# Kernel optimization log

Hardware: AMD Instinct MI355X
Metric: run time of the kernel (lower is better)

## Reference

```python
import jax, jax.numpy as jnp
import numpy as np

WINDOW_SIZE = 5
SIGMA = 1.5


def gaussian_kernel_3d(size, sigma):
    # Faithful replication of the torch code (including its permute quirk):
    # kernel[i,j,k] = exp(-((k-off)^2 + (k-off)^2 + (i-off)^2) / (2*sigma^2))
    c = jnp.arange(size, dtype=jnp.float32) - size // 2
    ci = c[:, None, None]  # axis 0 term (from permute(2,0,1))
    ck = c[None, None, :]  # axis 2 term (coords and permute(1,0,2) coincide)
    g = jnp.exp(-(ck ** 2 + ck ** 2 + ci ** 2) / (2.0 * sigma ** 2))
    g = jnp.broadcast_to(g, (size, size, size))
    return g / g.sum()


def _conv3d(x, w, pad):
    # x: [N,C,D,H,W], w: [O,I,kd,kh,kw]
    return jax.lax.conv_general_dilated(
        x, w, window_strides=(1, 1, 1),
        padding=[(pad, pad)] * 3,
        dimension_numbers=('NCDHW', 'OIDHW', 'NCDHW'))


def setup_inputs() -> dict:
    key = jax.random.key(0)
    k1, k2 = jax.random.split(key)
    img1 = jax.random.uniform(k1, (4, 2, 128, 128, 128), dtype=jnp.float32)
    img2 = jax.random.uniform(k2, (4, 1, 128, 128, 128), dtype=jnp.float32)
    window = gaussian_kernel_3d(WINDOW_SIZE, SIGMA)[None, None]  # [1,1,5,5,5]
    return {"img1": img1, "img2": img2, "window": window}


def reference(img1, img2, window):
    ws = window.shape[-1]
    pad = ws // 2
    x1 = img1[:, 1:2]  # select channel 1, keep dim -> [B,1,D,H,W]
    x2 = img2
    mu1 = _conv3d(x1, window, pad)
    mu2 = _conv3d(x2, window, pad)
    mu1_sq = mu1 * mu1
    mu2_sq = mu2 * mu2
    mu1_mu2 = mu1 * mu2
    sigma1_sq = _conv3d(x1 * x1, window, pad) - mu1_sq
    sigma2_sq = _conv3d(x2 * x2, window, pad) - mu2_sq
    sigma12 = _conv3d(x1 * x2, window, pad) - mu1_mu2
    C1 = 0.01 ** 2
    C2 = 0.03 ** 2
    ssim_map = ((2.0 * mu1_mu2 + C1) * (2.0 * sigma12 + C2)) / (
        (mu1_sq + mu2_sq + C1) * (sigma1_sq + sigma2_sq + C2))
    return 1.0 - jnp.mean(ssim_map)
```

## Files before the change

### kernel.cpp

```cpp
#include <hip/hip_runtime.h>


#define NDIM 128
#define TH 4
#define WR (TH + 4)
#define DSUB 16
#define NHT (NDIM / TH)
#define NDT (NDIM / DSUB)
#define NB 4
#define NBLK (NHT * NDT * NB)

__global__ void factorize_window(const float* __restrict__ w, float* __restrict__ ws) {
    if (threadIdx.x == 0) {
        float w000 = w[0];
        #pragma unroll
        for (int i = 0; i < 5; ++i) ws[i]      = w[i * 25];
        #pragma unroll
        for (int j = 0; j < 5; ++j) ws[5 + j]  = w[j * 5] / w000;
        #pragma unroll
        for (int k = 0; k < 5; ++k) ws[10 + k] = w[k] / w000;
    }
}

__launch_bounds__(256, 4)
__global__ void ssim_main(const float* __restrict__ img1,
                          const float* __restrict__ img2,
                          const float* __restrict__ wfac,
                          float* __restrict__ partials) {
    const int bid = blockIdx.x;
    const int th = bid % NHT;
    const int td = (bid / NHT) % NDT;
    const int b  = bid / (NHT * NDT);

    const int h0 = th * TH, d0 = td * DSUB;
    const float* __restrict__ x1 = img1 + (size_t)(b * 2 + 1) * NDIM * NDIM * NDIM;
    const float* __restrict__ x2 = img2 + (size_t)b * NDIM * NDIM * NDIM;

    float uW[5], vW[5], tW[5];
    #pragma unroll
    for (int i = 0; i < 5; ++i) { uW[i] = wfac[i]; vW[i] = wfac[5 + i]; tW[i] = wfac[10 + i]; }

    __shared__ float sWc[5][WR][NDIM];
    __shared__ float sRed[4];

    const int tid  = threadIdx.x;
    const int wrow = tid >> 5;
    const int wcg  = tid & 31;
    const int c0   = wcg * 4;
    const int ghw  = h0 + wrow - 2;
    const int orow = tid >> 6;
    const int oc   = (tid & 63) * 2;

    float2 ring[5][5];
    float2 accS = make_float2(0.f, 0.f);

#define PHASE(I, P) do {                                                       \
    const int i_ = (I);                                                        \
    const int d_ = d0 - 2 + i_;                                                \
    float4 A0 = make_float4(0,0,0,0), A1 = A0, A2 = A0;                        \
    float4 B0 = A0, B1 = A0, B2 = A0;                                          \
    if (((unsigned)d_ < NDIM) && ((unsigned)ghw < NDIM)) {                     \
        const float* __restrict__ r1_ = x1 + ((size_t)d_ * NDIM + ghw) * NDIM; \
        const float* __restrict__ r2_ = x2 + ((size_t)d_ * NDIM + ghw) * NDIM; \
        if (wcg > 0)  { A0 = *(const float4*)(r1_ + c0 - 4);                   \
                        B0 = *(const float4*)(r2_ + c0 - 4); }                 \
        A1 = *(const float4*)(r1_ + c0);                                       \
        B1 = *(const float4*)(r2_ + c0);                                       \
        if (wcg < 31) { A2 = *(const float4*)(r1_ + c0 + 4);                   \
                        B2 = *(const float4*)(r2_ + c0 + 4); }                 \
    }                                                                          \
    float ra[12] = {A0.x,A0.y,A0.z,A0.w, A1.x,A1.y,A1.z,A1.w,                  \
                    A2.x,A2.y,A2.z,A2.w};                                      \
    float rb[12] = {B0.x,B0.y,B0.z,B0.w, B1.x,B1.y,B1.z,B1.w,                  \
                    B2.x,B2.y,B2.z,B2.w};                                      \
    float m1v[4], m2v[4], q11v[4], q22v[4], q12v[4];                           \
    _Pragma("unroll")                                                          \
    for (int k_ = 0; k_ < 4; ++k_) {                                           \
        float m1_=0.f, m2_=0.f, q11_=0.f, q22_=0.f, q12_=0.f;                  \
        _Pragma("unroll")                                                      \
        for (int c_ = 0; c_ < 5; ++c_) {                                       \
            const float a_ = ra[k_ + c_ + 2], b_ = rb[k_ + c_ + 2];            \
            const float ta_ = tW[c_] * a_, tb_ = tW[c_] * b_;                  \
            m1_ += ta_; m2_ += tb_;                                            \
            q11_ += ta_ * a_; q22_ += tb_ * b_; q12_ += ta_ * b_;              \
        }                                                                      \
        m1v[k_]=m1_; m2v[k_]=m2_; q11v[k_]=q11_; q22v[k_]=q22_; q12v[k_]=q12_; \
    }                                                                          \
    __syncthreads();                   \
    *(float4*)&sWc[0][wrow][c0] = make_float4(m1v[0],m1v[1],m1v[2],m1v[3]);    \
    *(float4*)&sWc[1][wrow][c0] = make_float4(m2v[0],m2v[1],m2v[2],m2v[3]);    \
    *(float4*)&sWc[2][wrow][c0] = make_float4(q11v[0],q11v[1],q11v[2],q11v[3]);\
    *(float4*)&sWc[3][wrow][c0] = make_float4(q22v[0],q22v[1],q22v[2],q22v[3]);\
    *(float4*)&sWc[4][wrow][c0] = make_float4(q12v[0],q12v[1],q12v[2],q12v[3]);\
    __syncthreads();                                       \
    _Pragma("unroll")                                                          \
    for (int f_ = 0; f_ < 5; ++f_) {                                           \
        float2 F_ = make_float2(0.f, 0.f);                                     \
        _Pragma("unroll")                                                      \
        for (int r_ = 0; r_ < 5; ++r_) {                                       \
            const float2 wv_ = *(const float2*)&sWc[f_][orow + r_][oc];        \
            F_.x += vW[r_] * wv_.x;                                            \
            F_.y += vW[r_] * wv_.y;                                            \
        }                                                                      \
        ring[(P)][f_] = F_;                                                    \
    }                                                                          \
    if (i_ >= 4) {                                                             \
        float2 F0 = make_float2(0,0), F1 = F0, F2 = F0, F3 = F0, F4 = F0;      \
        _Pragma("unroll")                                                      \
        for (int j_ = 0; j_ < 5; ++j_) {                                       \
            const int s_ = ((P) + 1 + j_) % 5;                                 \
            const float uw_ = uW[j_];                                          \
            F0.x += uw_*ring[s_][0].x; F0.y += uw_*ring[s_][0].y;              \
            F1.x += uw_*ring[s_][1].x; F1.y += uw_*ring[s_][1].y;              \
            F2.x += uw_*ring[s_][2].x; F2.y += uw_*ring[s_][2].y;              \
            F3.x += uw_*ring[s_][3].x; F3.y += uw_*ring[s_][3].y;              \
            F4.x += uw_*ring[s_][4].x; F4.y += uw_*ring[s_][4].y;              \
        }                                                                      \
        {                                                                      \
            const float mu1 = F0.x, mu2 = F1.x;                                \
            const float m11 = mu1*mu1, m22 = mu2*mu2, m12 = mu1*mu2;           \
            const float num = (2.f*m12 + 1e-4f) * (2.f*(F4.x - m12) + 9e-4f);  \
            const float den = (m11 + m22 + 1e-4f) *                            \
                              ((F2.x - m11) + (F3.x - m22) + 9e-4f);           \
            accS.x += __fdividef(num, den);                                    \
        }                                                                      \
        {                                                                      \
            const float mu1 = F0.y, mu2 = F1.y;                                \
            const float m11 = mu1*mu1, m22 = mu2*mu2, m12 = mu1*mu2;           \
            const float num = (2.f*m12 + 1e-4f) * (2.f*(F4.y - m12) + 9e-4f);  \
            const float den = (m11 + m22 + 1e-4f) *                            \
                              ((F2.y - m11) + (F3.y - m22) + 9e-4f);           \
            accS.y += __fdividef(num, den);                                    \
        }                                                                      \
    }                                                                          \
} while (0)

    for (int io = 0; io < 4; ++io) {
        const int ib = io * 5;
        PHASE(ib + 0, 0);
        PHASE(ib + 1, 1);
        PHASE(ib + 2, 2);
        PHASE(ib + 3, 3);
        PHASE(ib + 4, 4);
    }
#undef PHASE

    float acc = accS.x + accS.y;
    #pragma unroll
    for (int off = 32; off > 0; off >>= 1)
        acc += __shfl_down(acc, off, 64);
    __syncthreads();
    if ((tid & 63) == 0) sRed[tid >> 6] = acc;
    __syncthreads();
    if (tid == 0) partials[bid] = sRed[0] + sRed[1] + sRed[2] + sRed[3];
}

__global__ void finalize_kernel(const float* __restrict__ partials, float* __restrict__ out) {
    const int tid = threadIdx.x;
    double s = 0.0;
    for (int i = tid; i < NBLK; i += 256) s += (double)partials[i];
    #pragma unroll
    for (int off = 32; off > 0; off >>= 1)
        s += __shfl_down(s, off, 64);
    __shared__ double sm[4];
    if ((tid & 63) == 0) sm[tid >> 6] = s;
    __syncthreads();
    if (tid == 0)
        out[0] = 1.0f - (float)((sm[0] + sm[1] + sm[2] + sm[3]) / (double)(4LL * 128 * 128 * 128));
}

extern "C" void kernel_launch(void* const* d_in, const int* in_sizes, int n_in,
                              void* d_out, int out_size, void* d_ws, size_t ws_size,
                              hipStream_t stream) {
    const float* img1 = (const float*)d_in[0];
    const float* img2 = (const float*)d_in[1];
    const float* win  = (const float*)d_in[2];
    float* out = (float*)d_out;
    float* ws  = (float*)d_ws;
    float* wfac     = ws;
    float* partials = ws + 16;

    hipLaunchKernelGGL(factorize_window, dim3(1), dim3(64), 0, stream, win, wfac);
    hipLaunchKernelGGL(ssim_main, dim3(NBLK), dim3(256), 0, stream, img1, img2, wfac, partials);
    hipLaunchKernelGGL(finalize_kernel, dim3(1), dim3(256), 0, stream, partials, out);
}
```

Before: 162.8 us.

## Split W dimension into two 64-wide tiles per block

Adds a width tiling so each block handles 64 columns instead of 128, doubling the block count. Each thread now loads float2 instead of float4 and computes two W-filtered outputs. The H pass runs only on half the threads (tid<128). The aim is more blocks for better occupancy and latency hiding. In exchange, halo reads across tile boundaries become redundant and half the threads sit idle in the H/D stage.

```diff
diff --git a/kernel.cpp b/kernel.cpp
--- a/kernel.cpp
+++ b/kernel.cpp
@@ -2,13 +2,15 @@
 
 
 #define NDIM 128
+#define TW64 64
 #define TH 4
 #define WR (TH + 4)
 #define DSUB 16
+#define NWT 2
 #define NHT (NDIM / TH)
 #define NDT (NDIM / DSUB)
 #define NB 4
-#define NBLK (NHT * NDT * NB)
+#define NBLK (NWT * NHT * NDT * NB)
 
 __global__ void factorize_window(const float* __restrict__ w, float* __restrict__ ws) {
     if (threadIdx.x == 0) {
@@ -28,11 +30,13 @@
                           const float* __restrict__ wfac,
                           float* __restrict__ partials) {
     const int bid = blockIdx.x;
-    const int th = bid % NHT;
-    const int td = (bid / NHT) % NDT;
-    const int b  = bid / (NHT * NDT);
+    const int tw = bid % NWT;
+    int t1 = bid / NWT;
+    const int th = t1 % NHT; t1 /= NHT;
+    const int td = t1 % NDT;
+    const int b  = t1 / NDT;
 
-    const int h0 = th * TH, d0 = td * DSUB;
+    const int w0 = tw * TW64, h0 = th * TH, d0 = td * DSUB;
     const float* __restrict__ x1 = img1 + (size_t)(b * 2 + 1) * NDIM * NDIM * NDIM;
     const float* __restrict__ x2 = img2 + (size_t)b * NDIM * NDIM * NDIM;
 
@@ -40,16 +44,20 @@
     #pragma unroll
     for (int i = 0; i < 5; ++i) { uW[i] = wfac[i]; vW[i] = wfac[5 + i]; tW[i] = wfac[10 + i]; }
 
-    __shared__ float sWc[5][WR][NDIM];
+    __shared__ float sWc[5][WR][TW64];
     __shared__ float sRed[4];
 
     const int tid  = threadIdx.x;
     const int wrow = tid >> 5;
     const int wcg  = tid & 31;
-    const int c0   = wcg * 4;
+    const int lc0  = wcg * 2;
+    const int gc0  = w0 + lc0;
     const int ghw  = h0 + wrow - 2;
-    const int orow = tid >> 6;
-    const int oc   = (tid & 63) * 2;
+    const bool haveL = (gc0 >= 2);
+    const bool haveR = (gc0 <= 124);
+    const bool active = (tid < 128);
+    const int orow = tid >> 5;
+    const int oc   = (tid & 31) * 2;
 
     float2 ring[5][5];
     float2 accS = make_float2(0.f, 0.f);
@@ -57,29 +65,27 @@
 #define PHASE(I, P) do {                                                       \
     const int i_ = (I);                                                        \
     const int d_ = d0 - 2 + i_;                                                \
-    float4 A0 = make_float4(0,0,0,0), A1 = A0, A2 = A0;                        \
-    float4 B0 = A0, B1 = A0, B2 = A0;                                          \
+    float2 A0 = make_float2(0,0), A1 = A0, A2 = A0;                            \
+    float2 B0 = A0, B1 = A0, B2 = A0;                                          \
     if (((unsigned)d_ < NDIM) && ((unsigned)ghw < NDIM)) {                     \
         const float* __restrict__ r1_ = x1 + ((size_t)d_ * NDIM + ghw) * NDIM; \
         const float* __restrict__ r2_ = x2 + ((size_t)d_ * NDIM + ghw) * NDIM; \
-        if (wcg > 0)  { A0 = *(const float4*)(r1_ + c0 - 4);                   \
-                        B0 = *(const float4*)(r2_ + c0 - 4); }                 \
-        A1 = *(const float4*)(r1_ + c0);                                       \
-        B1 = *(const float4*)(r2_ + c0);                                       \
-        if (wcg < 31) { A2 = *(const float4*)(r1_ + c0 + 4);                   \
-                        B2 = *(const float4*)(r2_ + c0 + 4); }                 \
+        if (haveL) { A0 = *(const float2*)(r1_ + gc0 - 2);                     \
+                     B0 = *(const float2*)(r2_ + gc0 - 2); }                   \
+        A1 = *(const float2*)(r1_ + gc0);                                      \
+        B1 = *(const float2*)(r2_ + gc0);                                      \
+        if (haveR) { A2 = *(const float2*)(r1_ + gc0 + 2);                     \
+                     B2 = *(const float2*)(r2_ + gc0 + 2); }                   \
     }                                                                          \
-    float ra[12] = {A0.x,A0.y,A0.z,A0.w, A1.x,A1.y,A1.z,A1.w,                  \
-                    A2.x,A2.y,A2.z,A2.w};                                      \
-    float rb[12] = {B0.x,B0.y,B0.z,B0.w, B1.x,B1.y,B1.z,B1.w,                  \
-                    B2.x,B2.y,B2.z,B2.w};                                      \
-    float m1v[4], m2v[4], q11v[4], q22v[4], q12v[4];                           \
+    float ra[6] = {A0.x, A0.y, A1.x, A1.y, A2.x, A2.y};                        \
+    float rb[6] = {B0.x, B0.y, B1.x, B1.y, B2.x, B2.y};                        \
+    float m1v[2], m2v[2], q11v[2], q22v[2], q12v[2];                           \
     _Pragma("unroll")                                                          \
-    for (int k_ = 0; k_ < 4; ++k_) {                                           \
+    for (int k_ = 0; k_ < 2; ++k_) {                                           \
         float m1_=0.f, m2_=0.f, q11_=0.f, q22_=0.f, q12_=0.f;                  \
         _Pragma("unroll")                                                      \
         for (int c_ = 0; c_ < 5; ++c_) {                                       \
-            const float a_ = ra[k_ + c_ + 2], b_ = rb[k_ + c_ + 2];            \
+            const float a_ = ra[k_ + c_], b_ = rb[k_ + c_];                    \
             const float ta_ = tW[c_] * a_, tb_ = tW[c_] * b_;                  \
             m1_ += ta_; m2_ += tb_;                                            \
             q11_ += ta_ * a_; q22_ += tb_ * b_; q12_ += ta_ * b_;              \
@@ -87,50 +93,52 @@
         m1v[k_]=m1_; m2v[k_]=m2_; q11v[k_]=q11_; q22v[k_]=q22_; q12v[k_]=q12_; \
     }                                                                          \
     __syncthreads();                   \
-    *(float4*)&sWc[0][wrow][c0] = make_float4(m1v[0],m1v[1],m1v[2],m1v[3]);    \
-    *(float4*)&sWc[1][wrow][c0] = make_float4(m2v[0],m2v[1],m2v[2],m2v[3]);    \
-    *(float4*)&sWc[2][wrow][c0] = make_float4(q11v[0],q11v[1],q11v[2],q11v[3]);\
-    *(float4*)&sWc[3][wrow][c0] = make_float4(q22v[0],q22v[1],q22v[2],q22v[3]);\
-    *(float4*)&sWc[4][wrow][c0] = make_float4(q12v[0],q12v[1],q12v[2],q12v[3]);\
+    *(float2*)&sWc[0][wrow][lc0] = make_float2(m1v[0], m1v[1]);                \
+    *(float2*)&sWc[1][wrow][lc0] = make_float2(m2v[0], m2v[1]);                \
+    *(float2*)&sWc[2][wrow][lc0] = make_float2(q11v[0], q11v[1]);              \
+    *(float2*)&sWc[3][wrow][lc0] = make_float2(q22v[0], q22v[1]);              \
+    *(float2*)&sWc[4][wrow][lc0] = make_float2(q12v[0], q12v[1]);              \
     __syncthreads();                                       \
-    _Pragma("unroll")                                                          \
-    for (int f_ = 0; f_ < 5; ++f_) {                                           \
-        float2 F_ = make_float2(0.f, 0.f);                                     \
+    if (active) {                                                              \
         _Pragma("unroll")                                                      \
-        for (int r_ = 0; r_ < 5; ++r_) {                                       \
-            const float2 wv_ = *(const float2*)&sWc[f_][orow + r_][oc];        \
-            F_.x += vW[r_] * wv_.x;                                            \
-            F_.y += vW[r_] * wv_.y;                                            \
+        for (int f_ = 0; f_ < 5; ++f_) {                                       \
+            float2 F_ = make_float2(0.f, 0.f);                                 \
+            _Pragma("unroll")                                                  \
+            for (int r_ = 0; r_ < 5; ++r_) {                                   \
+                const float2 wv_ = *(const float2*)&sWc[f_][orow + r_][oc];    \
+                F_.x += vW[r_] * wv_.x;                                        \
+                F_.y += vW[r_] * wv_.y;                                        \
+            }                                                                  \
+            ring[(P)][f_] = F_;                                                \
         }                                                                      \
-        ring[(P)][f_] = F_;                                                    \
-    }                                                                          \
-    if (i_ >= 4) {                                                             \
-        float2 F0 = make_float2(0,0), F1 = F0, F2 = F0, F3 = F0, F4 = F0;      \
-        _Pragma("unroll")                                                      \
-        for (int j_ = 0; j_ < 5; ++j_) {                                       \
-            const int s_ = ((P) + 1 + j_) % 5;                                 \
-            const float uw_ = uW[j_];                                          \
-            F0.x += uw_*ring[s_][0].x; F0.y += uw_*ring[s_][0].y;              \
-            F1.x += uw_*ring[s_][1].x; F1.y += uw_*ring[s_][1].y;              \
-            F2.x += uw_*ring[s_][2].x; F2.y += uw_*ring[s_][2].y;              \
-            F3.x += uw_*ring[s_][3].x; F3.y += uw_*ring[s_][3].y;              \
-            F4.x += uw_*ring[s_][4].x; F4.y += uw_*ring[s_][4].y;              \
-        }                                                                      \
-        {                                                                      \
-            const float mu1 = F0.x, mu2 = F1.x;                                \
-            const float m11 = mu1*mu1, m22 = mu2*mu2, m12 = mu1*mu2;           \
-            const float num = (2.f*m12 + 1e-4f) * (2.f*(F4.x - m12) + 9e-4f);  \
-            const float den = (m11 + m22 + 1e-4f) *                            \
-                              ((F2.x - m11) + (F3.x - m22) + 9e-4f);           \
-            accS.x += __fdividef(num, den);                                    \
-        }                                                                      \
-        {                                                                      \
-            const float mu1 = F0.y, mu2 = F1.y;                                \
-            const float m11 = mu1*mu1, m22 = mu2*mu2, m12 = mu1*mu2;           \
-            const float num = (2.f*m12 + 1e-4f) * (2.f*(F4.y - m12) + 9e-4f);  \
-            const float den = (m11 + m22 + 1e-4f) *                            \
-                              ((F2.y - m11) + (F3.y - m22) + 9e-4f);           \
-            accS.y += __fdividef(num, den);                                    \
+        if (i_ >= 4) {                                                         \
+            float2 F0 = make_float2(0,0), F1 = F0, F2 = F0, F3 = F0, F4 = F0;  \
+            _Pragma("unroll")                                                  \
+            for (int j_ = 0; j_ < 5; ++j_) {                                   \
+                const int s_ = ((P) + 1 + j_) % 5;                             \
+                const float uw_ = uW[j_];                                      \
+                F0.x += uw_*ring[s_][0].x; F0.y += uw_*ring[s_][0].y;          \
+                F1.x += uw_*ring[s_][1].x; F1.y += uw_*ring[s_][1].y;          \
+                F2.x += uw_*ring[s_][2].x; F2.y += uw_*ring[s_][2].y;          \
+                F3.x += uw_*ring[s_][3].x; F3.y += uw_*ring[s_][3].y;          \
+                F4.x += uw_*ring[s_][4].x; F4.y += uw_*ring[s_][4].y;          \
+            }                                                                  \
+            {                                                                  \
+                const float mu1 = F0.x, mu2 = F1.x;                            \
+                const float m11 = mu1*mu1, m22 = mu2*mu2, m12 = mu1*mu2;       \
+                const float num = (2.f*m12 + 1e-4f)*(2.f*(F4.x - m12) + 9e-4f);\
+                const float den = (m11 + m22 + 1e-4f) *                        \
+                                  ((F2.x - m11) + (F3.x - m22) + 9e-4f);       \
+                accS.x += __fdividef(num, den);                                \
+            }                                                                  \
+            {                                                                  \
+                const float mu1 = F0.y, mu2 = F1.y;                            \
+                const float m11 = mu1*mu1, m22 = mu2*mu2, m12 = mu1*mu2;       \
+                const float num = (2.f*m12 + 1e-4f)*(2.f*(F4.y - m12) + 9e-4f);\
+                const float den = (m11 + m22 + 1e-4f) *                        \
+                                  ((F2.y - m11) + (F3.y - m22) + 9e-4f);       \
+                accS.y += __fdividef(num, den);                                \
+            }                                                                  \
         }                                                                      \
     }                                                                          \
 } while (0)
```

Result: slower. 184.9 us (+13.6%).
